# Optimization experiments

Hardware: AMD Instinct MI355X
Metric: run time of the kernel (lower is better)

## Reference

```python
import jax, jax.numpy as jnp
import numpy as np

D_MODEL = 768
N_HEAD = 12
D_K = D_MODEL // N_HEAD
B, S = 2, 2048


def setup_inputs() -> dict:
    key = jax.random.key(0)
    ks = jax.random.split(key, 13)
    scale = 1.0 / np.sqrt(D_MODEL)
    inp = {
        'q': jax.random.normal(ks[0], (B, S, D_MODEL), jnp.float32),
        'k': jax.random.normal(ks[1], (B, S, D_MODEL), jnp.float32),
        'v': jax.random.normal(ks[2], (B, S, D_MODEL), jnp.float32),
        'Wq': jax.random.normal(ks[3], (D_MODEL, D_MODEL), jnp.float32) * scale,
        'bq': jnp.zeros((D_MODEL,), jnp.float32),
        'Wk': jax.random.normal(ks[4], (D_MODEL, D_MODEL), jnp.float32) * scale,
        'bk': jnp.zeros((D_MODEL,), jnp.float32),
        'Wv': jax.random.normal(ks[5], (D_MODEL, D_MODEL), jnp.float32) * scale,
        'bv': jnp.zeros((D_MODEL,), jnp.float32),
        'Wo': jax.random.normal(ks[6], (D_MODEL, D_MODEL), jnp.float32) * scale,
        'bo': jnp.zeros((D_MODEL,), jnp.float32),
        'mask': jax.random.randint(ks[7], (B, 1, S), 0, 2, jnp.int32),
    }
    return inp


def reference(q, k, v, Wq, bq, Wk, bk, Wv, bv, Wo, bo, mask):
    # project and split heads: [B,S,D] -> [B,H,S,Dk]
    def heads(x, W, b):
        y = x @ W + b
        return y.reshape(B, S, N_HEAD, D_K).transpose(0, 2, 1, 3)

    qh = heads(q, Wq, bq)
    kh = heads(k, Wk, bk)
    vh = heads(v, Wv, bv)
    # full score matrix [B,H,S,S] (intentionally materialized, as in source)
    scores = jnp.einsum('bhqd,bhkd->bhqk', qh, kh) / jnp.sqrt(jnp.float32(D_K))
    m = mask[:, None, :, :]  # [B,1,1,S] broadcast over heads and queries
    scores = jnp.where(m == 0, jnp.float32(-1e9), scores)
    p_attn = jax.nn.softmax(scores, axis=-1)
    # dropout omitted (eval / deterministic reference)
    x = jnp.einsum('bhqk,bhkd->bhqd', p_attn, vh)
    x = x.transpose(0, 2, 1, 3).reshape(B, S, D_MODEL)
    return x @ Wo + bo
```

## Files before the change

kernel.cpp:

```cpp
#include <hip/hip_runtime.h>


#define H_ 12
#define DK_ 64
#define B_DIM 2
#define SEQ 2048
#define DM 768
#define MROWS 4096
#define PER_IN ((size_t)MROWS * DM)
#define QSCALE 0.18033688011112042f

typedef short bf16x8 __attribute__((ext_vector_type(8)));
typedef short bf16x4 __attribute__((ext_vector_type(4)));
typedef float f32x4 __attribute__((ext_vector_type(4)));
typedef float f32x16 __attribute__((ext_vector_type(16)));

__device__ inline unsigned short f2bf(float f) {
    union { float f; unsigned int i; } x; x.f = f;
    unsigned int r = x.i + 0x7fff + ((x.i >> 16) & 1);
    return (unsigned short)(r >> 16);
}

__device__ inline unsigned pack2bf(float lo, float hi) {
#if __has_builtin(__builtin_amdgcn_cvt_pk_bf16_f32)
    auto v = __builtin_amdgcn_cvt_pk_bf16_f32(lo, hi);
    return __builtin_bit_cast(unsigned, v);
#else
    return (unsigned)f2bf(lo) | ((unsigned)f2bf(hi) << 16);
#endif
}

__device__ inline float exp2fast(float x) {
#if __has_builtin(__builtin_amdgcn_exp2f)
    return __builtin_amdgcn_exp2f(x);
#else
    return exp2f(x);
#endif
}

__device__ inline f32x16 mfma32x8(bf16x4 a, bf16x4 b, f32x16 c) {
#if __has_builtin(__builtin_amdgcn_mfma_f32_32x32x8bf16_1k)
    return __builtin_amdgcn_mfma_f32_32x32x8bf16_1k(a, b, c, 0, 0, 0);
#else
    asm("v_mfma_f32_32x32x8_bf16 %0, %1, %2, %0" : "+v"(c) : "v"(a), "v"(b));
    return c;
#endif
}

__device__ inline void gload_lds16(const unsigned short* g, unsigned short* ldsbase,
                                   int lane) {
#if __has_builtin(__builtin_amdgcn_global_load_lds)
    __builtin_amdgcn_global_load_lds(
        (const __attribute__((address_space(1))) unsigned int*)g,
        (__attribute__((address_space(3))) unsigned int*)ldsbase, 16, 0, 0);
#else
    *(uint4*)(ldsbase + 8 * lane) = *(const uint4*)g;
#endif
}

__global__ __launch_bounds__(256) void prep(
    const float* __restrict__ q, const float* __restrict__ k,
    const float* __restrict__ v,
    unsigned short* __restrict__ qb, unsigned short* __restrict__ kb,
    unsigned short* __restrict__ vb,
    const float* __restrict__ w0, const float* __restrict__ w1,
    const float* __restrict__ w2, const float* __restrict__ w3,
    unsigned short* __restrict__ wtbase,
    const int* __restrict__ mask, int* __restrict__ idx,
    int* __restrict__ nkeys) {
    __shared__ unsigned short t[32][33];
    __shared__ int wsum[4];
    int job = blockIdx.x, tid = threadIdx.x;
    if (job < 4608) {
        int buf = job / 1536, x = job % 1536;
        const float* src = buf == 0 ? q : (buf == 1 ? k : v);
        unsigned short* dst = buf == 0 ? qb : (buf == 1 ? kb : vb);
        size_t i = ((size_t)x * 256 + tid) * 8;
        float4 f0 = *(const float4*)(src + i);
        float4 f1 = *(const float4*)(src + i + 4);
        ushort4 u0, u1;
        u0.x = f2bf(f0.x); u0.y = f2bf(f0.y); u0.z = f2bf(f0.z); u0.w = f2bf(f0.w);
        u1.x = f2bf(f1.x); u1.y = f2bf(f1.y); u1.z = f2bf(f1.z); u1.w = f2bf(f1.w);
        *(ushort4*)(dst + i) = u0;
        *(ushort4*)(dst + i + 4) = u1;
    } else if (job < 6912) {
        int tb = job - 4608;
        int z = tb / 576, r = tb % 576, by = r / 24, bx = r % 24;
        const float* in = z == 0 ? w0 : (z == 1 ? w1 : (z == 2 ? w2 : w3));
        unsigned short* out = wtbase + (size_t)z * DM * DM;
        int x = tid & 31, y = tid >> 5;
        int k0 = bx * 32, n0 = by * 32;
#pragma unroll
        for (int i = 0; i < 32; i += 8)
            t[y + i][x] = f2bf(in[(size_t)(k0 + y + i) * DM + n0 + x]);
        __syncthreads();
#pragma unroll
        for (int i = 0; i < 32; i += 8)
            out[(size_t)(n0 + y + i) * DM + k0 + x] = t[x][y + i];
    } else {
        int b = job - 6912;
        int lane = tid & 63, wave = tid >> 6;
        const int* mp = mask + (size_t)b * SEQ + tid * 8;
        int4 a = *(const int4*)mp;
        int4 c = *(const int4*)(mp + 4);
        int m[8] = {a.x, a.y, a.z, a.w, c.x, c.y, c.z, c.w};
        int pre[8], s = 0;
#pragma unroll
        for (int e = 0; e < 8; e++) { pre[e] = s; s += (m[e] != 0); }
        int incl = s;
#pragma unroll
        for (int off = 1; off < 64; off <<= 1) {
            int vv = __shfl_up(incl, off);
            if (lane >= off) incl += vv;
        }
        int lexcl = incl - s;
        if (lane == 63) wsum[wave] = incl;
        __syncthreads();
        int base = lexcl;
        for (int w = 0; w < wave; w++) base += wsum[w];
#pragma unroll
        for (int e = 0; e < 8; e++)
            if (m[e]) idx[b * SEQ + base + pre[e]] = tid * 8 + e;
        if (tid == 0) nkeys[b] = wsum[0] + wsum[1] + wsum[2] + wsum[3];
    }
}

__global__ __launch_bounds__(256) void gatherKV(const unsigned short* __restrict__ Kh,
                                                const unsigned short* __restrict__ Vn,
                                                const int* __restrict__ idx,
                                                const int* __restrict__ nkeys,
                                                unsigned short* __restrict__ Kc,
                                                unsigned short* __restrict__ Vtc) {
    __shared__ unsigned short Tl[64][72];
    int tid = threadIdx.x;
    int j0 = blockIdx.x * 64, bh = blockIdx.y, b = bh / H_;
    int n = nkeys[b];
    int row = tid >> 2, cb = (tid & 3) * 16;
    int j = j0 + row;
    int src = j < n ? idx[b * SEQ + j] : -1;
    unsigned short v[16];
    unsigned short* ok = Kc + ((size_t)bh * SEQ + j) * DK_ + cb;
    if (src >= 0) {
        const unsigned short* gv = Vn + ((size_t)bh * SEQ + src) * DK_ + cb;
        *(uint4*)&v[0] = *(const uint4*)gv;
        *(uint4*)&v[8] = *(const uint4*)(gv + 8);
        const unsigned short* gk = Kh + ((size_t)bh * SEQ + src) * DK_ + cb;
        uint4 k0 = *(const uint4*)gk;
        uint4 k1 = *(const uint4*)(gk + 8);
        *(uint4*)ok = k0;
        *(uint4*)(ok + 8) = k1;
    } else {
        uint4 z = {0u, 0u, 0u, 0u};
        *(uint4*)&v[0] = z;
        *(uint4*)&v[8] = z;
        *(uint4*)ok = z;
        *(uint4*)(ok + 8) = z;
    }
#pragma unroll
    for (int e = 0; e < 16; e++)
        Tl[cb + e][row] = v[e];
    __syncthreads();
    uint4 o0 = *(const uint4*)&Tl[row][cb];
    uint4 o1 = *(const uint4*)&Tl[row][cb + 8];
    unsigned short* out = Vtc + ((size_t)bh * DK_ + row) * SEQ + j0 + cb;
    *(uint4*)out = o0;
    *(uint4*)(out + 8) = o1;
}

template <int QKV, int TM>
__global__ __launch_bounds__(256) void gemm128(
    const unsigned short* __restrict__ A0, const unsigned short* __restrict__ A1,
    const unsigned short* __restrict__ A2, const unsigned short* __restrict__ Wt,
    const float* __restrict__ bias0, const float* __restrict__ bias1,
    const float* __restrict__ bias2,
    void* __restrict__ O0, void* __restrict__ O1, void* __restrict__ O2) {
    __shared__ unsigned short S[2][TM + 128][64];
    const int K = DM;
    const int NT = K / 64;
    constexpr int NI = TM / 32;
    constexpr int AC = TM / 32;
    int tid = threadIdx.x;
    int wave = tid >> 6, lane = tid & 63, quad = lane >> 4, l15 = lane & 15;
    int wr = wave >> 1, wc = wave & 1;

    int nwg = gridDim.x * gridDim.y;
    int lin = blockIdx.y * gridDim.x + blockIdx.x;
    int swz = (lin & 7) * (nwg >> 3) + (lin >> 3);
    int bx = swz % gridDim.x, by = swz / gridDim.x;
    int m0 = bx * TM, n0 = by * 128;
    int lrow = lane >> 3, lcol = (lane & 7) * 8;

    int mi = 0, nb0 = n0;
    const unsigned short* A = A0;
    const float* bias = bias0;
    void* O = O0;
    if constexpr (QKV) {
        mi = n0 >= 1536 ? 2 : (n0 >= 768 ? 1 : 0);
        nb0 = n0 - mi * 768;
        A = mi == 0 ? A0 : (mi == 1 ? A1 : A2);
        bias = mi == 0 ? bias0 : (mi == 1 ? bias1 : bias2);
        O = mi == 0 ? O0 : (mi == 1 ? O1 : O2);
    }

    f32x4 acc[NI][4];
#pragma unroll
    for (int i = 0; i < NI; i++)
#pragma unroll
        for (int j = 0; j < 4; j++)
#pragma unroll
            for (int r = 0; r < 4; r++) acc[i][j][r] = 0.f;

    const unsigned short* gA = A + (size_t)(m0 + (TM / 4) * wave + lrow) * K + lcol;
    const unsigned short* gB = Wt + (size_t)(n0 + 32 * wave + lrow) * K + lcol;

#pragma unroll
    for (int c = 0; c < AC; c++)
        gload_lds16(gA + (size_t)8 * c * K, &S[0][(TM / 4) * wave + 8 * c][0], lane);
#pragma unroll
    for (int c = 0; c < 4; c++)
        gload_lds16(gB + (size_t)8 * c * K, &S[0][TM + 32 * wave + 8 * c][0], lane);

    for (int t = 0; t < NT; t++) {
        int cur = t & 1;
        if (t + 1 < NT) {
            int k0 = (t + 1) * 64;
#pragma unroll
            for (int c = 0; c < AC; c++)
                gload_lds16(gA + (size_t)8 * c * K + k0, &S[cur ^ 1][(TM / 4) * wave + 8 * c][0], lane);
#pragma unroll
            for (int c = 0; c < 4; c++)
                gload_lds16(gB + (size_t)8 * c * K + k0, &S[cur ^ 1][TM + 32 * wave + 8 * c][0], lane);
            if constexpr (TM == 128)
                asm volatile("s_waitcnt vmcnt(8)" ::: "memory");
            else
                asm volatile("s_waitcnt vmcnt(6)" ::: "memory");
        } else {
            asm volatile("s_waitcnt vmcnt(0)" ::: "memory");
        }
        __builtin_amdgcn_s_barrier();

        unsigned short (*Sl)[64] = S[cur];
#pragma unroll
        for (int ks = 0; ks < 64; ks += 32) {
            bf16x8 af[NI], bfr[4];
#pragma unroll
            for (int i = 0; i < NI; i++)
                af[i] = *(const bf16x8*)&Sl[(TM / 2) * wr + 16 * i + l15][ks + 8 * quad];
#pragma unroll
            for (int j = 0; j < 4; j++)
                bfr[j] = *(const bf16x8*)&Sl[TM + 64 * wc + 16 * j + l15][ks + 8 * quad];
#pragma unroll
            for (int i = 0; i < NI; i++)
#pragma unroll
                for (int j = 0; j < 4; j++)
                    acc[i][j] = __builtin_amdgcn_mfma_f32_16x16x32_bf16(af[i], bfr[j], acc[i][j], 0, 0, 0);
        }
        asm volatile("" ::: "memory");
        __builtin_amdgcn_s_barrier();
    }

    if constexpr (!QKV) {
#pragma unroll
        for (int j = 0; j < 4; j++) {
            int nn = nb0 + 64 * wc + 16 * j + l15;
            float bv = bias[nn];
#pragma unroll
            for (int i = 0; i < NI; i++)
#pragma unroll
                for (int r = 0; r < 4; r++) {
                    int m = m0 + (TM / 2) * wr + 16 * i + 4 * quad + r;
                    ((float*)O0)[(size_t)m * DM + nn] = acc[i][j][r] + bv;
                }
        }
    } else {
        float sc = mi == 0 ? QSCALE : 1.0f;
        __syncthreads();
        unsigned short (*Cl)[128] = (unsigned short(*)[128])S;
#pragma unroll
        for (int j = 0; j < 4; j++) {
            float bv = bias[nb0 + 64 * wc + 16 * j + l15];
#pragma unroll
            for (int i = 0; i < NI; i++)
#pragma unroll
                for (int r = 0; r < 4; r++)
                    Cl[(TM / 2) * wr + 16 * i + 4 * quad + r][64 * wc + 16 * j + l15] =
                        f2bf((acc[i][j][r] + bv) * sc);
        }
        __syncthreads();
        int row = tid >> 1, half = tid & 1;
        int m = m0 + row;
        int b = m >> 11, s = m & 2047;
        int h = (nb0 + 64 * half) >> 6;
        unsigned short* og = (unsigned short*)O + ((size_t)(b * H_ + h) * SEQ + s) * DK_;
        const unsigned short* cr = &Cl[row][64 * half];
#pragma unroll
        for (int c = 0; c < 4; c++)
            *(uint4*)(og + 16 * c) = *(const uint4*)(cr + 16 * c);
#pragma unroll
        for (int c = 0; c < 4; c++)
            *(uint4*)(og + 16 * c + 8) = *(const uint4*)(cr + 16 * c + 8);
    }
}

__global__ __launch_bounds__(256) void attn_fa(const unsigned short* __restrict__ Q,
                                               const unsigned short* __restrict__ Kc,
                                               const unsigned short* __restrict__ Vtc,
                                               const int* __restrict__ nkeys,
                                               unsigned short* __restrict__ ctx) {
    __shared__ __align__(16) unsigned short Ql[64][72];
    __shared__ __align__(16) unsigned short Kl[64][72];
    __shared__ __align__(16) unsigned short Vl[64][68];
    __shared__ __align__(16) float Op[2][32][32];
    __shared__ __align__(16) float lp[2][32];
    int tid = threadIdx.x;
    int wave = tid >> 6, lane = tid & 63;
    int l31 = lane & 31, hi = lane >> 5;
    int qh = wave & 1, kh = wave >> 1;
    int bh = blockIdx.y, b = bh / H_, h = bh % H_;
    int q0 = blockIdx.x * 64;

    int n = nkeys[b];
    int nt = (n + 63) >> 6;
    float padf = (float)(nt * 64 - n);

    {
        int row = tid >> 2, cb = (tid & 3) * 16;
        const unsigned short* gq = Q + ((size_t)bh * SEQ + q0 + row) * DK_ + cb;
        *(uint4*)&Ql[row][cb]     = *(const uint4*)gq;
        *(uint4*)&Ql[row][cb + 8] = *(const uint4*)(gq + 8);
    }
    __syncthreads();

    bf16x8 qf[4];
#pragma unroll
    for (int c = 0; c < 4; c++)
        qf[c] = *(const bf16x8*)&Ql[32 * qh + l31][16 * c + 8 * hi];

    union { unsigned u[2]; bf16x4 v; } onesu;
    onesu.u[0] = 0x3F803F80u; onesu.u[1] = 0x3F803F80u;
    bf16x4 ones = onesu.v;

    f32x16 o[2][2];
    f32x16 lsum;
#pragma unroll
    for (int r = 0; r < 16; r++) lsum[r] = 0.f;
#pragma unroll
    for (int dt = 0; dt < 2; dt++)
#pragma unroll
        for (int p = 0; p < 2; p++)
#pragma unroll
            for (int r = 0; r < 16; r++) o[dt][p][r] = 0.f;

    int krow = tid >> 2, kcb = (tid & 3) * 16;
    const unsigned short* gk = Kc + ((size_t)bh * SEQ + krow) * DK_ + kcb;
    const unsigned short* gv = Vtc + ((size_t)bh * DK_ + krow) * SEQ + kcb;

    uint4 kr0 = *(const uint4*)gk, kr1 = *(const uint4*)(gk + 8);
    uint4 vr0 = *(const uint4*)gv, vr1 = *(const uint4*)(gv + 8);

    for (int kt = 0; kt < nt; kt++) {
        __syncthreads();
        *(uint4*)&Kl[krow][kcb]     = kr0;
        *(uint4*)&Kl[krow][kcb + 8] = kr1;
        *(uint4*)&Vl[krow][kcb]     = vr0;
        *(uint4*)&Vl[krow][kcb + 8] = vr1;
        __syncthreads();
        if (kt + 1 < nt) {
            gk += (size_t)64 * DK_;
            gv += 64;
            kr0 = *(const uint4*)gk; kr1 = *(const uint4*)(gk + 8);
            vr0 = *(const uint4*)gv; vr1 = *(const uint4*)(gv + 8);
        }

        f32x16 sT;
#pragma unroll
        for (int r = 0; r < 16; r++) sT[r] = 0.f;
#pragma unroll
        for (int c = 0; c < 4; c++) {
            bf16x8 kf = *(const bf16x8*)&Kl[32 * kh + l31][16 * c + 8 * hi];
            sT = __builtin_amdgcn_mfma_f32_32x32x16_bf16(kf, qf[c], sT, 0, 0, 0);
        }

        bf16x4 pfrag[4];
#pragma unroll
        for (int c = 0; c < 4; c++) {
            float p0 = exp2fast(sT[4 * c + 0]);
            float p1 = exp2fast(sT[4 * c + 1]);
            float p2 = exp2fast(sT[4 * c + 2]);
            float p3 = exp2fast(sT[4 * c + 3]);
            union { unsigned u[2]; bf16x4 v; } pk;
            pk.u[0] = pack2bf(p0, p1);
            pk.u[1] = pack2bf(p2, p3);
            pfrag[c] = pk.v;
        }

#pragma unroll
        for (int c = 0; c < 4; c++)
            lsum = mfma32x8(pfrag[c], ones, lsum);

#pragma unroll
        for (int dt = 0; dt < 2; dt++)
#pragma unroll
            for (int c = 0; c < 4; c++) {
                bf16x4 vf = *(const bf16x4*)&Vl[32 * dt + l31][32 * kh + 8 * c + 4 * hi];
                o[dt][c & 1] = mfma32x8(pfrag[c], vf, o[dt][c & 1]);
            }
    }

#pragma unroll
    for (int dt = 0; dt < 2; dt++) {
        if (kh == 1) {
#pragma unroll
            for (int r = 0; r < 16; r++) {
                int qrl = (r & 3) + 8 * (r >> 2) + 4 * hi;
                Op[qh][qrl][l31] = o[dt][0][r] + o[dt][1][r];
                if (dt == 0 && l31 == 0) lp[qh][qrl] = lsum[r];
            }
        }
        __syncthreads();
        if (kh == 0) {
#pragma unroll
            for (int r = 0; r < 16; r++) {
                int qrl = (r & 3) + 8 * (r >> 2) + 4 * hi;
                float l = lsum[r] + lp[qh][qrl] - padf;
                float iv = l > 0.f ? 1.f / l : 0.f;
                int qg = q0 + 32 * qh + qrl;
                size_t base = ((size_t)b * SEQ + qg) * DM + h * DK_;
                float v = o[dt][0][r] + o[dt][1][r] + Op[qh][qrl][l31];
                ctx[base + 32 * dt + l31] = f2bf(v * iv);
            }
        }
        __syncthreads();
    }
}

extern "C" void kernel_launch(void* const* d_in, const int* in_sizes, int n_in,
                              void* d_out, int out_size, void* d_ws, size_t ws_size,
                              hipStream_t stream) {
    const float* q  = (const float*)d_in[0];
    const float* k  = (const float*)d_in[1];
    const float* v  = (const float*)d_in[2];
    const float* Wq = (const float*)d_in[3];
    const float* bq = (const float*)d_in[4];
    const float* Wk = (const float*)d_in[5];
    const float* bk = (const float*)d_in[6];
    const float* Wv = (const float*)d_in[7];
    const float* bv = (const float*)d_in[8];
    const float* Wo = (const float*)d_in[9];
    const float* bo = (const float*)d_in[10];
    const int* mask = (const int*)d_in[11];

    unsigned short* ws = (unsigned short*)d_ws;
    unsigned short* qb = ws;
    unsigned short* kb = ws + PER_IN;
    unsigned short* vb = ws + 2 * PER_IN;
    unsigned short* Qh = ws + 3 * PER_IN;
    unsigned short* Kh = ws + 4 * PER_IN;
    unsigned short* Vhn = ws + 5 * PER_IN;
    unsigned short* WtQKV = ws + 6 * PER_IN;
    unsigned short* WtO = WtQKV + (size_t)3 * DM * DM;
    unsigned short* Kc = kb;
    unsigned short* Vtc = vb;
    unsigned short* ctx = qb;
    int* idx = (int*)d_out;
    int* nk = idx + B_DIM * SEQ;

    prep<<<dim3(6914), 256, 0, stream>>>(q, k, v, qb, kb, vb,
                                         Wq, Wk, Wv, Wo, WtQKV, mask, idx, nk);

    gemm128<1, 128><<<dim3(MROWS / 128, 3 * DM / 128), 256, 0, stream>>>(
        qb, kb, vb, WtQKV, bq, bk, bv, Qh, Kh, Vhn);

    gatherKV<<<dim3(SEQ / 64, B_DIM * H_), 256, 0, stream>>>(Kh, Vhn, idx, nk, Kc, Vtc);

    attn_fa<<<dim3(SEQ / 64, B_DIM * H_), 256, 0, stream>>>(Qh, Kc, Vtc, nk, ctx);

    gemm128<0, 64><<<dim3(MROWS / 64, DM / 128), 256, 0, stream>>>(
        ctx, ctx, ctx, WtO, bo, bo, bo, d_out, d_out, d_out);
}
```

Before: 197.2 us.

## Scatter K/V rows into compacted order from QKV GEMM epilogue

The mask prefix scan now produces a destination position per key (valid keys first, masked keys after), and the QKV projection epilogue writes K and V rows straight to those compacted positions. The gather kernel therefore no longer copies K; it only transposes the compacted V and zeroes K padding up to the next multiple of 64. This removes one full read and write of K and an indirect index lookup, in exchange for scattered row writes in the GEMM epilogue.

```diff
diff --git a/kernel.cpp b/kernel.cpp
--- a/kernel.cpp
+++ b/kernel.cpp
@@ -66,7 +66,7 @@
     const float* __restrict__ w0, const float* __restrict__ w1,
     const float* __restrict__ w2, const float* __restrict__ w3,
     unsigned short* __restrict__ wtbase,
-    const int* __restrict__ mask, int* __restrict__ idx,
+    const int* __restrict__ mask, int* __restrict__ pos,
     int* __restrict__ nkeys) {
     __shared__ unsigned short t[32][33];
     __shared__ int wsum[4];
@@ -118,43 +118,42 @@
         __syncthreads();
         int base = lexcl;
         for (int w = 0; w < wave; w++) base += wsum[w];
-#pragma unroll
-        for (int e = 0; e < 8; e++)
-            if (m[e]) idx[b * SEQ + base + pre[e]] = tid * 8 + e;
-        if (tid == 0) nkeys[b] = wsum[0] + wsum[1] + wsum[2] + wsum[3];
-    }
-}
-
-__global__ __launch_bounds__(256) void gatherKV(const unsigned short* __restrict__ Kh,
-                                                const unsigned short* __restrict__ Vn,
-                                                const int* __restrict__ idx,
-                                                const int* __restrict__ nkeys,
-                                                unsigned short* __restrict__ Kc,
-                                                unsigned short* __restrict__ Vtc) {
+        int nq = wsum[0] + wsum[1] + wsum[2] + wsum[3];
+#pragma unroll
+        for (int e = 0; e < 8; e++) {
+            int sidx = tid * 8 + e;
+            int rk = base + pre[e];
+            pos[b * SEQ + sidx] = m[e] ? rk : (nq + sidx - rk);
+        }
+        if (tid == 0) nkeys[b] = nq;
+    }
+}
+
+__global__ __launch_bounds__(256) void gatherV(const unsigned short* __restrict__ Vc,
+                                               const int* __restrict__ nkeys,
+                                               unsigned short* __restrict__ Kc,
+                                               unsigned short* __restrict__ Vtc) {
     __shared__ unsigned short Tl[64][72];
     int tid = threadIdx.x;
     int j0 = blockIdx.x * 64, bh = blockIdx.y, b = bh / H_;
     int n = nkeys[b];
+    int npad = (n + 63) & ~63;
     int row = tid >> 2, cb = (tid & 3) * 16;
     int j = j0 + row;
-    int src = j < n ? idx[b * SEQ + j] : -1;
     unsigned short v[16];
-    unsigned short* ok = Kc + ((size_t)bh * SEQ + j) * DK_ + cb;
-    if (src >= 0) {
-        const unsigned short* gv = Vn + ((size_t)bh * SEQ + src) * DK_ + cb;
+    if (j < n) {
+        const unsigned short* gv = Vc + ((size_t)bh * SEQ + j) * DK_ + cb;
         *(uint4*)&v[0] = *(const uint4*)gv;
         *(uint4*)&v[8] = *(const uint4*)(gv + 8);
-        const unsigned short* gk = Kh + ((size_t)bh * SEQ + src) * DK_ + cb;
-        uint4 k0 = *(const uint4*)gk;
-        uint4 k1 = *(const uint4*)(gk + 8);
-        *(uint4*)ok = k0;
-        *(uint4*)(ok + 8) = k1;
     } else {
         uint4 z = {0u, 0u, 0u, 0u};
         *(uint4*)&v[0] = z;
         *(uint4*)&v[8] = z;
-        *(uint4*)ok = z;
-        *(uint4*)(ok + 8) = z;
+        if (j < npad) {
+            unsigned short* ok = Kc + ((size_t)bh * SEQ + j) * DK_ + cb;
+            *(uint4*)ok = z;
+            *(uint4*)(ok + 8) = z;
+        }
     }
 #pragma unroll
     for (int e = 0; e < 16; e++)
@@ -173,6 +172,7 @@
     const unsigned short* __restrict__ A2, const unsigned short* __restrict__ Wt,
     const float* __restrict__ bias0, const float* __restrict__ bias1,
     const float* __restrict__ bias2,
+    const int* __restrict__ pos,
     void* __restrict__ O0, void* __restrict__ O1, void* __restrict__ O2) {
     __shared__ unsigned short S[2][TM + 128][64];
     const int K = DM;
@@ -290,8 +290,9 @@
         int row = tid >> 1, half = tid & 1;
         int m = m0 + row;
         int b = m >> 11, s = m & 2047;
+        int j = (mi == 0) ? s : pos[b * SEQ + s];
         int h = (nb0 + 64 * half) >> 6;
-        unsigned short* og = (unsigned short*)O + ((size_t)(b * H_ + h) * SEQ + s) * DK_;
+        unsigned short* og = (unsigned short*)O + ((size_t)(b * H_ + h) * SEQ + j) * DK_;
         const unsigned short* cr = &Cl[row][64 * half];
 #pragma unroll
         for (int c = 0; c < 4; c++)
@@ -455,26 +456,25 @@
     unsigned short* kb = ws + PER_IN;
     unsigned short* vb = ws + 2 * PER_IN;
     unsigned short* Qh = ws + 3 * PER_IN;
-    unsigned short* Kh = ws + 4 * PER_IN;
-    unsigned short* Vhn = ws + 5 * PER_IN;
+    unsigned short* Kc = ws + 4 * PER_IN;
+    unsigned short* Vc = ws + 5 * PER_IN;
     unsigned short* WtQKV = ws + 6 * PER_IN;
     unsigned short* WtO = WtQKV + (size_t)3 * DM * DM;
-    unsigned short* Kc = kb;
     unsigned short* Vtc = vb;
     unsigned short* ctx = qb;
-    int* idx = (int*)d_out;
-    int* nk = idx + B_DIM * SEQ;
+    int* pos = (int*)d_out;
+    int* nk = pos + B_DIM * SEQ;
 
     prep<<<dim3(6914), 256, 0, stream>>>(q, k, v, qb, kb, vb,
-                                         Wq, Wk, Wv, Wo, WtQKV, mask, idx, nk);
+                                         Wq, Wk, Wv, Wo, WtQKV, mask, pos, nk);
 
     gemm128<1, 128><<<dim3(MROWS / 128, 3 * DM / 128), 256, 0, stream>>>(
-        qb, kb, vb, WtQKV, bq, bk, bv, Qh, Kh, Vhn);
-
-    gatherKV<<<dim3(SEQ / 64, B_DIM * H_), 256, 0, stream>>>(Kh, Vhn, idx, nk, Kc, Vtc);
+        qb, kb, vb, WtQKV, bq, bk, bv, pos, Qh, Kc, Vc);
+
+    gatherV<<<dim3(SEQ / 64, B_DIM * H_), 256, 0, stream>>>(Vc, nk, Kc, Vtc);
 
     attn_fa<<<dim3(SEQ / 64, B_DIM * H_), 256, 0, stream>>>(Qh, Kc, Vtc, nk, ctx);
 
     gemm128<0, 64><<<dim3(MROWS / 64, DM / 128), 256, 0, stream>>>(
-        ctx, ctx, ctx, WtO, bo, bo, bo, d_out, d_out, d_out);
-}
+        ctx, ctx, ctx, WtO, bo, bo, bo, pos, d_out, d_out, d_out);
+}
```

New measurement: 195.3 us. About the same (-1.0%).
